# Kernel tuning notes

Hardware: AMD Instinct MI355X
Metric: run time of the kernel (lower is better)

## Reference

```python
import jax, jax.numpy as jnp
import numpy as np
import math

T, HW, M, D, DK, H, SIGMA = 16, 1024, 256, 768, 768, 8, 0.5
HD = DK // H
VHD = D // H
EPS = 1e-6
SCALE = 1.0 / math.sqrt(HD)


def _ln(x, g):
    # LayerNorm(eps=1e-6, bias=False)
    m = x.mean(-1, keepdims=True)
    v = ((x - m) ** 2).mean(-1, keepdims=True)
    return (x - m) / jnp.sqrt(v + EPS) * g


def setup_inputs() -> dict:
    key = jax.random.key(0)
    ks = jax.random.split(key, 16)
    s = 0.02
    features = jax.random.normal(ks[0], (T, HW, D), jnp.float32)
    tracks = jax.random.uniform(ks[1], (T, M, 2), jnp.float32)
    track_pos_embeddings = jax.random.normal(ks[2], (T, M, D), jnp.float32)
    feature_pos_embeddings = jax.random.normal(ks[3], (T, HW, D), jnp.float32)
    g = jnp.linspace(0.0, 1.0, 32)
    feature_positions = jnp.stack(jnp.meshgrid(g, g, indexing='ij'), axis=-1).reshape(HW, 2)
    return {
        'features': features,
        'tracks': tracks,
        'feature_positions': feature_positions,
        'track_pos_embeddings': track_pos_embeddings,
        'feature_pos_embeddings': feature_pos_embeddings,
        # AttentionalSampling params (nn.Linear weights are [out,in])
        'Wq_s': jax.random.normal(ks[4], (DK, D)) * s,
        'Wk_s': jax.random.normal(ks[5], (DK, D)) * s,
        'Wv_s': jax.random.normal(ks[6], (D, D)) * s,
        'qg_s': jnp.ones((DK,), jnp.float32),
        'kg_s': jnp.ones((DK,), jnp.float32),
        'Wo_s': jax.random.normal(ks[7], (D, D)) * s,
        # AttentionalSplatting params
        'Wq_p': jax.random.normal(ks[8], (DK, D)) * s,
        'Wk_p': jax.random.normal(ks[9], (DK, D)) * s,
        'Wv_p': jax.random.normal(ks[10], (D, D)) * s,
        'qg_p': jnp.ones((DK,), jnp.float32),
        'kg_p': jnp.ones((DK,), jnp.float32),
        'Wout_p': jax.random.normal(ks[11], (D, D)) * s,
    }


def reference(features, tracks, feature_positions, track_pos_embeddings,
              feature_pos_embeddings, Wq_s, Wk_s, Wv_s, qg_s, kg_s, Wo_s,
              Wq_p, Wk_p, Wv_p, qg_p, kg_p, Wout_p):
    # per-frame Gaussian spatial bias from squared euclidean distances
    # d2[t,m,n] = ||tracks[t,m] - feature_positions[n]||^2  -> [T, M, HW]
    d2 = ((tracks[:, :, None, :] - feature_positions[None, None, :, :]) ** 2).sum(-1)
    bias = -d2 / (2.0 * SIGMA ** 2)  # [T, M, HW]

    # ---- Attentional Sampling: tracks query features ----
    Q = _ln(track_pos_embeddings @ Wq_s.T, qg_s)          # [T, M, DK]
    K = _ln((features + feature_pos_embeddings) @ Wk_s.T, kg_s)  # [T, HW, DK]
    V = features @ Wv_s.T                                  # [T, HW, D]
    Qh = Q.reshape(T, M, H, HD).transpose(0, 2, 1, 3)      # [T, H, M, HD]
    Kh = K.reshape(T, HW, H, HD).transpose(0, 2, 1, 3)     # [T, H, HW, HD]
    Vh = V.reshape(T, HW, H, VHD).transpose(0, 2, 1, 3)    # [T, H, HW, VHD]
    scores = jnp.einsum('thmd,thnd->thmn', Qh, Kh) * SCALE + bias[:, None]
    A = jax.nn.softmax(scores, axis=-1)
    sampled = jnp.einsum('thmn,thnd->thmd', A, Vh)
    sampled = sampled.transpose(0, 2, 1, 3).reshape(T, M, D) @ Wo_s.T  # [T, M, D]

    # ---- Attentional Splatting: features query tracks ----
    Q2 = _ln(feature_pos_embeddings @ Wq_p.T, qg_p)        # [T, HW, DK]
    K2 = _ln(track_pos_embeddings @ Wk_p.T, kg_p)          # [T, M, DK]
    V2 = sampled @ Wv_p.T                                   # [T, M, D]
    Q2h = Q2.reshape(T, HW, H, HD).transpose(0, 2, 1, 3)   # [T, H, HW, HD]
    K2h = K2.reshape(T, M, H, HD).transpose(0, 2, 1, 3)    # [T, H, M, HD]
    V2h = V2.reshape(T, M, H, VHD).transpose(0, 2, 1, 3)   # [T, H, M, VHD]
    bias_t = jnp.swapaxes(bias, 1, 2)                       # [T, HW, M] (cdist is symmetric)
    scores2 = jnp.einsum('thnd,thmd->thnm', Q2h, K2h) * SCALE + bias_t[:, None]
    A2 = jax.nn.softmax(scores2, axis=-1)
    upd = jnp.einsum('thnm,thmd->thnd', A2, V2h)
    feature_updates = upd.transpose(0, 2, 1, 3).reshape(T, HW, D) @ Wout_p.T
    return features + feature_updates
```

## Files before the change

### kernel.cpp

```cpp
#include <hip/hip_runtime.h>

#define DD 768
#define HDIM 96
#define ATT_SCALE 0.10206207261596575f

typedef float floatx4 __attribute__((ext_vector_type(4)));
typedef __bf16 bf16;
typedef bf16 bf16x8 __attribute__((ext_vector_type(8)));
typedef bf16 bf16x4 __attribute__((ext_vector_type(4)));
typedef bf16 bf16x2 __attribute__((ext_vector_type(2)));

__device__ __forceinline__ void gl2lds16(const bf16* g, bf16* l) {
  __builtin_amdgcn_global_load_lds(
      (const __attribute__((address_space(1))) void*)g,
      (__attribute__((address_space(3))) void*)l, 16, 0, 0);
}

__global__ __launch_bounds__(256) void prep(
    const float* __restrict__ features, const float* __restrict__ fpe,
    const float* __restrict__ tpe,
    const float* w0, const float* w1, const float* w2, const float* w3,
    const float* w4, const float* w5, const float* w6, const float* w7,
    bf16* __restrict__ Fb, bf16* __restrict__ Xb, bf16* __restrict__ Feb,
    bf16* __restrict__ Tb, bf16* __restrict__ Wb, bf16* __restrict__ WoT) {
  const int b = blockIdx.x;
  const int tid = threadIdx.x;
  if (b < 6144) {
    const int i = (b * 256 + tid) * 8;
    floatx4 f0 = *(const floatx4*)(features + i);
    floatx4 f1 = *(const floatx4*)(features + i + 4);
    floatx4 e0 = *(const floatx4*)(fpe + i);
    floatx4 e1 = *(const floatx4*)(fpe + i + 4);
    bf16x8 fv, xv, ev;
#pragma unroll
    for (int k = 0; k < 4; k++) {
      fv[k] = (bf16)f0[k];           fv[k + 4] = (bf16)f1[k];
      ev[k] = (bf16)e0[k];           ev[k + 4] = (bf16)e1[k];
      xv[k] = (bf16)(f0[k] + e0[k]); xv[k + 4] = (bf16)(f1[k] + e1[k]);
    }
    *(bf16x8*)(Fb + i) = fv;
    *(bf16x8*)(Xb + i) = xv;
    *(bf16x8*)(Feb + i) = ev;
  } else if (b < 7680) {
    const int i = ((b - 6144) * 256 + tid) * 8;
    floatx4 s0 = *(const floatx4*)(tpe + i);
    floatx4 s1 = *(const floatx4*)(tpe + i + 4);
    bf16x8 v;
#pragma unroll
    for (int k = 0; k < 4; k++) { v[k] = (bf16)s0[k]; v[k + 4] = (bf16)s1[k]; }
    *(bf16x8*)(Tb + i) = v;
  } else if (b < 9984) {
    const int sub = b - 7680;
    const int wi = sub / 288, xb = sub % 288;
    const float* srcs[8] = {w0, w1, w2, w3, w4, w5, w6, w7};
    const float* s = srcs[wi];
    bf16* d = Wb + (size_t)wi * 589824;
    const int i = (xb * 256 + tid) * 8;
    floatx4 s0 = *(const floatx4*)(s + i);
    floatx4 s1 = *(const floatx4*)(s + i + 4);
    bf16x8 v;
#pragma unroll
    for (int k = 0; k < 4; k++) { v[k] = (bf16)s0[k]; v[k + 4] = (bf16)s1[k]; }
    *(bf16x8*)(d + i) = v;
  } else {
    __shared__ float Ts[64][65];
    const int sub = b - 9984;
    const int X0 = (sub % 12) * 64, Y0 = (sub / 12) * 64;
    const int r = tid >> 2;
    const int c4 = (tid & 3) * 16;
    const float* src = w3 + (size_t)(Y0 + r) * DD + X0 + c4;
#pragma unroll
    for (int k = 0; k < 16; k += 4) {
      floatx4 v = *(const floatx4*)(src + k);
      Ts[r][c4 + k] = v[0]; Ts[r][c4 + k + 1] = v[1];
      Ts[r][c4 + k + 2] = v[2]; Ts[r][c4 + k + 3] = v[3];
    }
    __syncthreads();
    bf16 o[16];
#pragma unroll
    for (int k = 0; k < 16; k++) o[k] = (bf16)Ts[c4 + k][r];
    *(bf16x8*)(WoT + (size_t)(X0 + r) * DD + Y0 + c4) = *(bf16x8*)&o[0];
    *(bf16x8*)(WoT + (size_t)(X0 + r) * DD + Y0 + c4 + 8) = *(bf16x8*)&o[8];
  }
}

__device__ __forceinline__ void ln_row(bf16* x, const float* g, int lane) {
  float v[12], s = 0.f, ss = 0.f;
#pragma unroll
  for (int j = 0; j < 3; j++) {
    bf16x4 b = *(const bf16x4*)&x[j * 256 + lane * 4];
#pragma unroll
    for (int e = 0; e < 4; e++) {
      float t = (float)b[e];
      v[j * 4 + e] = t; s += t; ss += t * t;
    }
  }
#pragma unroll
  for (int o = 32; o > 0; o >>= 1) { s += __shfl_xor(s, o); ss += __shfl_xor(ss, o); }
  const float mean = s * (1.0f / DD);
  const float inv = rsqrtf(ss * (1.0f / DD) - mean * mean + 1e-6f);
#pragma unroll
  for (int j = 0; j < 3; j++) {
    floatx4 gg = *(const floatx4*)&g[j * 256 + lane * 4];
    bf16x4 o4;
#pragma unroll
    for (int e = 0; e < 4; e++) o4[e] = (bf16)((v[j * 4 + e] - mean) * inv * gg[e]);
    *(bf16x4*)&x[j * 256 + lane * 4] = o4;
  }
}

__global__ __launch_bounds__(256) void ln_all(bf16* X0, const float* g0,
                                              bf16* X1, const float* g1,
                                              bf16* X2, const float* g2,
                                              bf16* X3, const float* g3) {
  const int b = blockIdx.x;
  bf16* X; const float* g; int base;
  if (b < 4096)      { X = X0; g = g0; base = b; }
  else if (b < 8192) { X = X1; g = g1; base = b - 4096; }
  else if (b < 9216) { X = X2; g = g2; base = b - 8192; }
  else               { X = X3; g = g3; base = b - 9216; }
  const int w = threadIdx.x >> 6, lane = threadIdx.x & 63;
  ln_row(X + (size_t)(base * 4 + w) * DD, g, lane);
}

template <int MODE>
__device__ __forceinline__ void gemm_core64(const bf16* __restrict__ A,
                                            const bf16* __restrict__ W,
                                            bf16* __restrict__ Cb,
                                            float* __restrict__ Cf,
                                            const float* __restrict__ addsrc,
                                            bf16* As, bf16* Ws,
                                            int row0, int col0) {
  const int tid = threadIdx.x;
  const int lane = tid & 63;
  const int w = tid >> 6;
  const int wm = (w & 1) * 64;
  const int wn = (w >> 1) * 64;
  const int fr = lane & 15;
  const int quad = lane >> 4;
  const int srow = tid >> 2;
  const int scol = (tid & 3) * 8;
  const bf16* Ag = A + (size_t)(row0 + srow) * DD + scol;
  const bf16* Wg = W + (size_t)(col0 + srow) * DD + scol;
  bf16* AsD = &As[tid * 8];
  bf16* WsD = &Ws[tid * 8];

  floatx4 acc[4][4];
#pragma unroll
  for (int i = 0; i < 4; i++)
#pragma unroll
    for (int j = 0; j < 4; j++) acc[i][j] = (floatx4){0, 0, 0, 0};

  for (int k0 = 0; k0 < DD; k0 += 64) {
    __syncthreads();
    gl2lds16(Ag + k0, AsD);
    gl2lds16(Ag + k0 + (size_t)64 * DD, AsD + 2048);
    gl2lds16(Wg + k0, WsD);
    gl2lds16(Wg + k0 + (size_t)64 * DD, WsD + 2048);
    gl2lds16(Ag + k0 + 32, AsD + 4096);
    gl2lds16(Ag + k0 + 32 + (size_t)64 * DD, AsD + 4096 + 2048);
    gl2lds16(Wg + k0 + 32, WsD + 4096);
    gl2lds16(Wg + k0 + 32 + (size_t)64 * DD, WsD + 4096 + 2048);
    __syncthreads();
#pragma unroll
    for (int half = 0; half < 2; half++) {
      const bf16* Ah = As + half * 4096;
      const bf16* Wh = Ws + half * 4096;
      bf16x8 af[4], bfr[4];
#pragma unroll
      for (int i = 0; i < 4; i++)
        af[i] = *(const bf16x8*)&Ah[(wm + i * 16 + fr) * 32 + quad * 8];
#pragma unroll
      for (int j = 0; j < 4; j++)
        bfr[j] = *(const bf16x8*)&Wh[(wn + j * 16 + fr) * 32 + quad * 8];
#pragma unroll
      for (int i = 0; i < 4; i++)
#pragma unroll
        for (int j = 0; j < 4; j++)
          acc[i][j] = __builtin_amdgcn_mfma_f32_16x16x32_bf16(af[i], bfr[j], acc[i][j], 0, 0, 0);
    }
  }
#pragma unroll
  for (int i = 0; i < 4; i++)
#pragma unroll
    for (int j = 0; j < 4; j++)
#pragma unroll
      for (int r = 0; r < 4; r++) {
        const int row = row0 + wm + i * 16 + quad * 4 + r;
        const int col = col0 + wn + j * 16 + fr;
        const size_t idx = (size_t)row * DD + col;
        if (MODE == 0) Cb[idx] = (bf16)acc[i][j][r];
        else Cf[idx] = acc[i][j][r] + addsrc[idx];
      }
}

__global__ __launch_bounds__(256) void gemm_all(
    const bf16* Xb, const bf16* Fb, const bf16* Feb, const bf16* Tb,
    const bf16* Wb, const bf16* WoT,
    bf16* Kc, bf16* Vc, bf16* Qb2, bf16* Qc, bf16* K2, bf16* Wcr) {
  __shared__ bf16 As[8192], Ws[8192];
  const size_t SW = (size_t)768 * 768;
  const int z = blockIdx.z;
  if (z == 0)
    gemm_core64<0>(Xb, Wb + 1 * SW, Kc, nullptr, nullptr, As, Ws,
                   blockIdx.x * 128, blockIdx.y * 128);
  else if (z == 1)
    gemm_core64<0>(Fb, Wb + 2 * SW, Vc, nullptr, nullptr, As, Ws,
                   blockIdx.x * 128, blockIdx.y * 128);
  else if (z == 2)
    gemm_core64<0>(Feb, Wb + 4 * SW, Qb2, nullptr, nullptr, As, Ws,
                   blockIdx.x * 128, blockIdx.y * 128);
  else {
    const int x = blockIdx.x;
    if (x < 32)
      gemm_core64<0>(Tb, Wb + 0 * SW, Qc, nullptr, nullptr, As, Ws,
                     x * 128, blockIdx.y * 128);
    else if (x < 64)
      gemm_core64<0>(Tb, Wb + 5 * SW, K2, nullptr, nullptr, As, Ws,
                     (x - 32) * 128, blockIdx.y * 128);
    else if (x < 70)
      gemm_core64<0>(Wb + 6 * SW, WoT, Wcr, nullptr, nullptr, As, Ws,
                     (x - 64) * 128, blockIdx.y * 128);
  }
}

__global__ __launch_bounds__(256) void gemm_b(const bf16* A, const bf16* W, bf16* C) {
  __shared__ bf16 As[8192], Ws[8192];
  gemm_core64<0>(A, W, C, nullptr, nullptr, As, Ws, blockIdx.x * 128, blockIdx.y * 128);
}

__global__ __launch_bounds__(256) void gemm_final(const bf16* A, const bf16* W,
                                                  float* C, const float* addsrc) {
  __shared__ bf16 As[8192], Ws[8192];
  gemm_core64<1>(A, W, nullptr, C, addsrc, As, Ws, blockIdx.x * 128, blockIdx.y * 128);
}

template <int SPLIT>
__global__ __launch_bounds__(512, 4) void attn512(
    const bf16* __restrict__ Qb, const bf16* __restrict__ Kb,
    const bf16* __restrict__ Vb, bf16* __restrict__ Ob,
    float* __restrict__ Ml,
    const float* __restrict__ qpos, int qpos_ts,
    const float* __restrict__ kpos, int kpos_ts,
    int nq, int nk, int npq, int nsp) {
  const int b = blockIdx.x;
  const int h = b & 7;
  const int t = (b >> 3) & 15;
  const int rest = b >> 7;
  const int qt = rest % npq;
  const int sp = rest / npq;
  const int klen = nk / nsp;
  const int k0s = sp * klen;
  const int q0 = qt * 128;
  const bf16* Q = Qb + (size_t)t * nq * DD + h * HDIM;
  const bf16* K = Kb + (size_t)t * nk * DD + h * HDIM;
  const bf16* V = Vb + (size_t)t * nk * DD + h * HDIM;
  bf16* O = Ob + (size_t)(SPLIT ? (sp * 16 + t) : t) * nq * DD + h * HDIM;
  const float* qp = qpos + (size_t)t * qpos_ts;
  const float* kp = kpos + (size_t)t * kpos_ts;

  __shared__ bf16 Ks[64 * 104];
  __shared__ bf16 Vt[96 * 72];
  __shared__ bf16 Ps[2 * 64 * 72];

  const int tid = threadIdx.x;
  const int w = tid >> 6;
  const int g = w >> 2;
  const int wl = w & 3;
  const int lane = tid & 63;
  const int fr = lane & 15;
  const int quad = lane >> 4;
  const int rowb = wl * 16;
  const int qgb = q0 + g * 64;
  bf16* Pg = &Ps[g * 64 * 72];

  bf16x8 qf[3];
  {
    const bf16* qrow = Q + (size_t)(qgb + rowb + fr) * DD;
#pragma unroll
    for (int c = 0; c < 3; c++) qf[c] = *(const bf16x8*)(qrow + c * 32 + quad * 8);
  }
  float qx[4], qy[4];
#pragma unroll
  for (int r = 0; r < 4; r++) {
    int qi = qgb + rowb + quad * 4 + r;
    qx[r] = qp[qi * 2];
    qy[r] = qp[qi * 2 + 1];
  }

  float lrow[4] = {0.f, 0.f, 0.f, 0.f};
  floatx4 oacc[6];
#pragma unroll
  for (int d = 0; d < 6; d++) oacc[d] = (floatx4){0, 0, 0, 0};

  const int krA = tid >> 3, kcA = (tid & 7) * 8;
  const int krB = (tid & 255) >> 2, kcB = 64 + (tid & 3) * 8;
  const int nb = (tid & 31) * 2, db = (tid >> 5) * 6;

  for (int n0 = k0s; n0 < k0s + klen; n0 += 64) {
    __syncthreads();
    *(bf16x8*)&Ks[krA * 104 + kcA] =
        *(const bf16x8*)(K + (size_t)(n0 + krA) * DD + kcA);
    if (tid < 256)
      *(bf16x8*)&Ks[krB * 104 + kcB] =
          *(const bf16x8*)(K + (size_t)(n0 + krB) * DD + kcB);
    {
      bf16 tmp[2][6];
#pragma unroll
      for (int nn = 0; nn < 2; nn++) {
        const unsigned* vg = (const unsigned*)(V + (size_t)(n0 + nb + nn) * DD + db);
        unsigned u0 = vg[0], u1 = vg[1], u2 = vg[2];
        *(unsigned*)&tmp[nn][0] = u0;
        *(unsigned*)&tmp[nn][2] = u1;
        *(unsigned*)&tmp[nn][4] = u2;
      }
#pragma unroll
      for (int dd = 0; dd < 6; dd++) {
        bf16x2 v2 = {tmp[0][dd], tmp[1][dd]};
        *(bf16x2*)&Vt[(db + dd) * 72 + nb] = v2;
      }
    }
    __syncthreads();

    floatx4 s4[4];
#pragma unroll
    for (int j = 0; j < 4; j++) {
      floatx4 sa = {0, 0, 0, 0};
#pragma unroll
      for (int c = 0; c < 3; c++) {
        bf16x8 kf = *(const bf16x8*)&Ks[(j * 16 + fr) * 104 + c * 32 + quad * 8];
        sa = __builtin_amdgcn_mfma_f32_16x16x32_bf16(qf[c], kf, sa, 0, 0, 0);
      }
      s4[j] = sa;
    }
    float kxx[4], kyy[4];
#pragma unroll
    for (int j = 0; j < 4; j++) {
      int ki = (n0 + j * 16 + fr) * 2;
      kxx[j] = kp[ki];
      kyy[j] = kp[ki + 1];
    }
#pragma unroll
    for (int j = 0; j < 4; j++)
#pragma unroll
      for (int r = 0; r < 4; r++) {
        float dx = qx[r] - kxx[j], dy = qy[r] - kyy[j];
        float sv = s4[j][r] * ATT_SCALE - 2.0f * (dx * dx + dy * dy);
        float pv = __expf(sv);
        lrow[r] += pv;
        Pg[(rowb + quad * 4 + r) * 72 + j * 16 + fr] = (bf16)pv;
      }
    bf16x8 pf0 = *(const bf16x8*)&Pg[(rowb + fr) * 72 + quad * 8];
    bf16x8 pf1 = *(const bf16x8*)&Pg[(rowb + fr) * 72 + 32 + quad * 8];
#pragma unroll
    for (int d = 0; d < 6; d++) {
      bf16x8 v0 = *(const bf16x8*)&Vt[(d * 16 + fr) * 72 + quad * 8];
      bf16x8 v1 = *(const bf16x8*)&Vt[(d * 16 + fr) * 72 + 32 + quad * 8];
      oacc[d] = __builtin_amdgcn_mfma_f32_16x16x32_bf16(pf0, v0, oacc[d], 0, 0, 0);
      oacc[d] = __builtin_amdgcn_mfma_f32_16x16x32_bf16(pf1, v1, oacc[d], 0, 0, 0);
    }
  }

#pragma unroll
  for (int r = 0; r < 4; r++)
#pragma unroll
    for (int o = 1; o < 16; o <<= 1) lrow[r] += __shfl_xor(lrow[r], o);

#pragma unroll
  for (int r = 0; r < 4; r++) {
    int row = qgb + rowb + quad * 4 + r;
    if (SPLIT) {
#pragma unroll
      for (int d = 0; d < 6; d++)
        O[(size_t)row * DD + d * 16 + fr] = (bf16)oacc[d][r];
      if (fr == 0)
        Ml[((size_t)(sp * 16 + t) * 8 + h) * nq + row] = lrow[r];
    } else {
      float inv = 1.0f / lrow[r];
#pragma unroll
      for (int d = 0; d < 6; d++)
        O[(size_t)row * DD + d * 16 + fr] = (bf16)(oacc[d][r] * inv);
    }
  }
}

__global__ __launch_bounds__(256) void combine4(const bf16* __restrict__ Op,
                                                const float* __restrict__ Ml,
                                                bf16* __restrict__ Out) {
  const int row = blockIdx.x;
  const int t = row >> 8;
  const int q = row & 255;
#pragma unroll
  for (int e = 0; e < 3; e++) {
    int dim = threadIdx.x + e * 256;
    int hh = dim / 96;
    float osum = 0.f, lsum = 0.f;
#pragma unroll
    for (int s = 0; s < 4; s++) {
      lsum += Ml[((size_t)(s * 16 + t) * 8 + hh) * 256 + q];
      osum += (float)Op[((size_t)(s * 16 + t) * 256 + q) * DD + dim];
    }
    Out[(size_t)row * DD + dim] = (bf16)(osum / lsum);
  }
}

extern "C" void kernel_launch(void* const* d_in, const int* in_sizes, int n_in,
                              void* d_out, int out_size, void* d_ws, size_t ws_size,
                              hipStream_t stream) {
  const float* features = (const float*)d_in[0];
  const float* tracks   = (const float*)d_in[1];
  const float* fpos     = (const float*)d_in[2];
  const float* tpe      = (const float*)d_in[3];
  const float* fpe      = (const float*)d_in[4];
  const float* Wq_s     = (const float*)d_in[5];
  const float* Wk_s     = (const float*)d_in[6];
  const float* Wv_s     = (const float*)d_in[7];
  const float* qg_s     = (const float*)d_in[8];
  const float* kg_s     = (const float*)d_in[9];
  const float* Wo_s     = (const float*)d_in[10];
  const float* Wq_p     = (const float*)d_in[11];
  const float* Wk_p     = (const float*)d_in[12];
  const float* Wv_p     = (const float*)d_in[13];
  const float* qg_p     = (const float*)d_in[14];
  const float* kg_p     = (const float*)d_in[15];
  const float* Wout_p   = (const float*)d_in[16];
  float* out = (float*)d_out;

  const size_t SB = (size_t)16 * 1024 * 768;
  const size_t SS = (size_t)16 * 256 * 768;
  const size_t SW = (size_t)768 * 768;
  bf16* p = (bf16*)d_ws;
  bf16* Fb  = p; p += SB;
  bf16* Xb  = p; p += SB;
  bf16* Feb = p; p += SB;
  bf16* Kc  = p; p += SB;
  bf16* Vc  = p; p += SB;
  bf16* Qb2 = p; p += SB;
  bf16* Tb  = p; p += SS;
  bf16* Qc  = p; p += SS;
  bf16* K2  = p; p += SS;
  bf16* Sh  = p; p += SS;
  bf16* Op  = p; p += 4 * SS;
  bf16* Wb  = p; p += 8 * SW;
  bf16* WoT = p; p += SW;
  bf16* Wcr = p; p += SW;
  float* Ml = (float*)p;
  bf16* V2 = Qc; bf16* U = Fb;

  dim3 blk(256);

  prep<<<10128, blk, 0, stream>>>(features, fpe, tpe,
                                  Wq_s, Wk_s, Wv_s, Wo_s, Wq_p, Wk_p, Wv_p, Wout_p,
                                  Fb, Xb, Feb, Tb, Wb, WoT);
  gemm_all<<<dim3(128, 6, 4), blk, 0, stream>>>(Xb, Fb, Feb, Tb, Wb, WoT,
                                                Kc, Vc, Qb2, Qc, K2, Wcr);
  ln_all<<<10240, blk, 0, stream>>>(Kc, kg_s, Qb2, qg_p, Qc, qg_s, K2, kg_p);
  attn512<1><<<1024, dim3(512), 0, stream>>>(Qc, Kc, Vc, Op, Ml,
                                             tracks, 512, fpos, 0, 256, 1024, 2, 4);
  combine4<<<4096, blk, 0, stream>>>(Op, Ml, Sh);
  gemm_b<<<dim3(32, 6), blk, 0, stream>>>(Sh, Wcr, V2);
  attn512<0><<<1024, dim3(512), 0, stream>>>(Qb2, K2, V2, U, nullptr,
                                             fpos, 0, tracks, 512, 1024, 256, 8, 1);
  gemm_final<<<dim3(128, 6), blk, 0, stream>>>(U, Wb + 7 * SW, out, features);
}
```

Before: 474.4 us.

## Replace 128x128 GEMM core with 256x256 double-buffered, swizzled 8-wave pipeline

Replaces the shared GEMM routine with a 256x256 output tile computed by 512 threads (8 waves). It double-buffers LDS staging with direct global-to-LDS loads and XOR-swizzles the LDS layout to avoid bank conflicts. An explicitly interleaved schedule of LDS fragment reads, MFMA bursts, barriers, vmcnt waits and setprio is meant to overlap global prefetch with matrix math and raise operand reuse per byte loaded. The cost is 128KB of LDS per block, so likely one block per CU, and far fewer blocks per GEMM (e.g. 192 for the final projection). That can leave CUs idle and gives less latency hiding from occupancy.

New measurement: 440.1 us. 1.08x faster.

```diff
diff --git a/kernel.cpp b/kernel.cpp
--- a/kernel.cpp
+++ b/kernel.cpp
@@ -123,116 +123,189 @@
   ln_row(X + (size_t)(base * 4 + w) * DD, g, lane);
 }
 
+#define BAR() do { __builtin_amdgcn_sched_barrier(0); \
+                   __builtin_amdgcn_s_barrier(); \
+                   __builtin_amdgcn_sched_barrier(0); } while (0)
+#define VMW(n) asm volatile("s_waitcnt vmcnt(" #n ")" ::: "memory")
+
 template <int MODE>
-__device__ __forceinline__ void gemm_core64(const bf16* __restrict__ A,
-                                            const bf16* __restrict__ W,
-                                            bf16* __restrict__ Cb,
-                                            float* __restrict__ Cf,
-                                            const float* __restrict__ addsrc,
-                                            bf16* As, bf16* Ws,
-                                            int row0, int col0) {
+__device__ __forceinline__ void gemm256(const bf16* __restrict__ A,
+                                        const bf16* __restrict__ W,
+                                        bf16* __restrict__ Cb,
+                                        float* __restrict__ Cf,
+                                        const float* __restrict__ addsrc,
+                                        bf16* lds, int row0, int col0) {
   const int tid = threadIdx.x;
   const int lane = tid & 63;
   const int w = tid >> 6;
-  const int wm = (w & 1) * 64;
+  const int wm = (w & 1) * 128;
   const int wn = (w >> 1) * 64;
   const int fr = lane & 15;
   const int quad = lane >> 4;
-  const int srow = tid >> 2;
-  const int scol = (tid & 3) * 8;
-  const bf16* Ag = A + (size_t)(row0 + srow) * DD + scol;
-  const bf16* Wg = W + (size_t)(col0 + srow) * DD + scol;
-  bf16* AsD = &As[tid * 8];
-  bf16* WsD = &Ws[tid * 8];
-
-  floatx4 acc[4][4];
-#pragma unroll
-  for (int i = 0; i < 4; i++)
+  const int f7 = fr & 7;
+
+  const int srow = tid >> 3;
+  const int sswz = ((tid & 7) ^ (srow & 7)) * 8;
+  const bf16* Ag = A + (size_t)(row0 + srow) * DD + sswz;
+  const bf16* Wg = W + (size_t)(col0 + srow) * DD + sswz;
+  bf16* dA = lds + tid * 8;
+  bf16* dB = lds + 32768 + tid * 8;
+
+#define STGA(tau, h) do { \
+    gl2lds16(Ag + (size_t)((h) * 128) * DD + (tau) * 64, \
+             dA + ((tau) & 1) * 16384 + (h) * 8192); \
+    gl2lds16(Ag + (size_t)((h) * 128 + 64) * DD + (tau) * 64, \
+             dA + ((tau) & 1) * 16384 + (h) * 8192 + 4096); \
+  } while (0)
+#define STGB(tau, h) do { \
+    gl2lds16(Wg + (size_t)((h) * 128) * DD + (tau) * 64, \
+             dB + ((tau) & 1) * 16384 + (h) * 8192); \
+    gl2lds16(Wg + (size_t)((h) * 128 + 64) * DD + (tau) * 64, \
+             dB + ((tau) & 1) * 16384 + (h) * 8192 + 4096); \
+  } while (0)
+
+  const int sl0 = (quad ^ f7) * 8;
+  const int sl1 = ((4 | quad) ^ f7) * 8;
+
+#define LDA8(buf, mh) do { \
+    _Pragma("unroll") for (int m = 0; m < 4; m++) { \
+      const bf16* p = lds + (buf) * 16384 + (wm + (mh) * 64 + m * 16 + fr) * 64; \
+      af[m][0] = *(const bf16x8*)(p + sl0); \
+      af[m][1] = *(const bf16x8*)(p + sl1); } \
+  } while (0)
+#define LDB4(buf, nh, dst) do { \
+    _Pragma("unroll") for (int n = 0; n < 2; n++) { \
+      const bf16* p = lds + 32768 + (buf) * 16384 + (wn + (nh) * 32 + n * 16 + fr) * 64; \
+      dst[n][0] = *(const bf16x8*)(p + sl0); \
+      dst[n][1] = *(const bf16x8*)(p + sl1); } \
+  } while (0)
+#define MM16(mh, nbase, bb) do { \
+    __builtin_amdgcn_s_setprio(1); \
+    _Pragma("unroll") for (int m = 0; m < 4; m++) \
+    _Pragma("unroll") for (int n = 0; n < 2; n++) { \
+      acc[(mh) * 4 + m][(nbase) + n] = __builtin_amdgcn_mfma_f32_16x16x32_bf16( \
+          af[m][0], bb[n][0], acc[(mh) * 4 + m][(nbase) + n], 0, 0, 0); \
+      acc[(mh) * 4 + m][(nbase) + n] = __builtin_amdgcn_mfma_f32_16x16x32_bf16( \
+          af[m][1], bb[n][1], acc[(mh) * 4 + m][(nbase) + n], 0, 0, 0); } \
+    __builtin_amdgcn_s_setprio(0); \
+  } while (0)
+
+  floatx4 acc[8][4];
+
+  STGB(0, 0); STGB(0, 1); STGA(0, 0); STGA(0, 1);
+  STGB(1, 0); STGB(1, 1);
+#pragma unroll
+  for (int i = 0; i < 8; i++)
 #pragma unroll
     for (int j = 0; j < 4; j++) acc[i][j] = (floatx4){0, 0, 0, 0};
-
-  for (int k0 = 0; k0 < DD; k0 += 64) {
-    __syncthreads();
-    gl2lds16(Ag + k0, AsD);
-    gl2lds16(Ag + k0 + (size_t)64 * DD, AsD + 2048);
-    gl2lds16(Wg + k0, WsD);
-    gl2lds16(Wg + k0 + (size_t)64 * DD, WsD + 2048);
-    gl2lds16(Ag + k0 + 32, AsD + 4096);
-    gl2lds16(Ag + k0 + 32 + (size_t)64 * DD, AsD + 4096 + 2048);
-    gl2lds16(Wg + k0 + 32, WsD + 4096);
-    gl2lds16(Wg + k0 + 32 + (size_t)64 * DD, WsD + 4096 + 2048);
-    __syncthreads();
-#pragma unroll
-    for (int half = 0; half < 2; half++) {
-      const bf16* Ah = As + half * 4096;
-      const bf16* Wh = Ws + half * 4096;
-      bf16x8 af[4], bfr[4];
-#pragma unroll
-      for (int i = 0; i < 4; i++)
-        af[i] = *(const bf16x8*)&Ah[(wm + i * 16 + fr) * 32 + quad * 8];
-#pragma unroll
-      for (int j = 0; j < 4; j++)
-        bfr[j] = *(const bf16x8*)&Wh[(wn + j * 16 + fr) * 32 + quad * 8];
-#pragma unroll
-      for (int i = 0; i < 4; i++)
-#pragma unroll
-        for (int j = 0; j < 4; j++)
-          acc[i][j] = __builtin_amdgcn_mfma_f32_16x16x32_bf16(af[i], bfr[j], acc[i][j], 0, 0, 0);
-    }
-  }
-#pragma unroll
-  for (int i = 0; i < 4; i++)
-#pragma unroll
-    for (int j = 0; j < 4; j++)
+  VMW(4);
+  BAR();
+
+  bf16x8 af[4][2], b0[2][2], b1[2][2];
+
+  for (int it = 0; it < 6; ++it) {
+    const int a = 2 * it;
+    const bool stg = (it < 5);
+    LDA8(0, 0); LDB4(0, 0, b0);
+    STGA(a + 1, 0);
+    BAR();
+    MM16(0, 0, b0);
+    BAR();
+    LDB4(0, 1, b1);
+    STGA(a + 1, 1);
+    BAR();
+    MM16(0, 2, b1);
+    BAR();
+    LDA8(0, 1);
+    if (stg) STGB(a + 2, 0);
+    BAR();
+    MM16(1, 2, b1);
+    BAR();
+    if (stg) STGB(a + 2, 1);
+    BAR();
+    MM16(1, 0, b0);
+    if (stg) { VMW(4); } else { VMW(0); }
+    BAR();
+    LDA8(1, 0); LDB4(1, 0, b0);
+    if (stg) STGA(a + 2, 0);
+    BAR();
+    MM16(0, 0, b0);
+    BAR();
+    LDB4(1, 1, b1);
+    if (stg) STGA(a + 2, 1);
+    BAR();
+    MM16(0, 2, b1);
+    BAR();
+    LDA8(1, 1);
+    if (stg) STGB(a + 3, 0);
+    BAR();
+    MM16(1, 2, b1);
+    BAR();
+    if (stg) STGB(a + 3, 1);
+    BAR();
+    MM16(1, 0, b0);
+    if (stg) VMW(4);
+    BAR();
+  }
+
+#pragma unroll
+  for (int m = 0; m < 8; m++)
+#pragma unroll
+    for (int n = 0; n < 4; n++)
 #pragma unroll
       for (int r = 0; r < 4; r++) {
-        const int row = row0 + wm + i * 16 + quad * 4 + r;
-        const int col = col0 + wn + j * 16 + fr;
+        const int row = row0 + wm + m * 16 + quad * 4 + r;
+        const int col = col0 + wn + n * 16 + fr;
         const size_t idx = (size_t)row * DD + col;
-        if (MODE == 0) Cb[idx] = (bf16)acc[i][j][r];
-        else Cf[idx] = acc[i][j][r] + addsrc[idx];
+        if (MODE == 0) Cb[idx] = (bf16)acc[m][n][r];
+        else Cf[idx] = acc[m][n][r] + addsrc[idx];
       }
-}
-
-__global__ __launch_bounds__(256) void gemm_all(
+#undef STGA
+#undef STGB
+#undef LDA8
+#undef LDB4
+#undef MM16
+}
+
+__global__ __launch_bounds__(512, 2) void gemm_all(
     const bf16* Xb, const bf16* Fb, const bf16* Feb, const bf16* Tb,
     const bf16* Wb, const bf16* WoT,
     bf16* Kc, bf16* Vc, bf16* Qb2, bf16* Qc, bf16* K2, bf16* Wcr) {
-  __shared__ bf16 As[8192], Ws[8192];
+  __shared__ bf16 lds[65536];
   const size_t SW = (size_t)768 * 768;
   const int z = blockIdx.z;
   if (z == 0)
-    gemm_core64<0>(Xb, Wb + 1 * SW, Kc, nullptr, nullptr, As, Ws,
-                   blockIdx.x * 128, blockIdx.y * 128);
+    gemm256<0>(Xb, Wb + 1 * SW, Kc, nullptr, nullptr, lds,
+               blockIdx.x * 256, blockIdx.y * 256);
   else if (z == 1)
-    gemm_core64<0>(Fb, Wb + 2 * SW, Vc, nullptr, nullptr, As, Ws,
-                   blockIdx.x * 128, blockIdx.y * 128);
+    gemm256<0>(Fb, Wb + 2 * SW, Vc, nullptr, nullptr, lds,
+               blockIdx.x * 256, blockIdx.y * 256);
   else if (z == 2)
-    gemm_core64<0>(Feb, Wb + 4 * SW, Qb2, nullptr, nullptr, As, Ws,
-                   blockIdx.x * 128, blockIdx.y * 128);
+    gemm256<0>(Feb, Wb + 4 * SW, Qb2, nullptr, nullptr, lds,
+               blockIdx.x * 256, blockIdx.y * 256);
   else {
     const int x = blockIdx.x;
-    if (x < 32)
-      gemm_core64<0>(Tb, Wb + 0 * SW, Qc, nullptr, nullptr, As, Ws,
-                     x * 128, blockIdx.y * 128);
-    else if (x < 64)
-      gemm_core64<0>(Tb, Wb + 5 * SW, K2, nullptr, nullptr, As, Ws,
-                     (x - 32) * 128, blockIdx.y * 128);
-    else if (x < 70)
-      gemm_core64<0>(Wb + 6 * SW, WoT, Wcr, nullptr, nullptr, As, Ws,
-                     (x - 64) * 128, blockIdx.y * 128);
-  }
-}
-
-__global__ __launch_bounds__(256) void gemm_b(const bf16* A, const bf16* W, bf16* C) {
-  __shared__ bf16 As[8192], Ws[8192];
-  gemm_core64<0>(A, W, C, nullptr, nullptr, As, Ws, blockIdx.x * 128, blockIdx.y * 128);
-}
-
-__global__ __launch_bounds__(256) void gemm_final(const bf16* A, const bf16* W,
-                                                  float* C, const float* addsrc) {
-  __shared__ bf16 As[8192], Ws[8192];
-  gemm_core64<1>(A, W, nullptr, C, addsrc, As, Ws, blockIdx.x * 128, blockIdx.y * 128);
+    if (x < 16)
+      gemm256<0>(Tb, Wb + 0 * SW, Qc, nullptr, nullptr, lds,
+                 x * 256, blockIdx.y * 256);
+    else if (x < 32)
+      gemm256<0>(Tb, Wb + 5 * SW, K2, nullptr, nullptr, lds,
+                 (x - 16) * 256, blockIdx.y * 256);
+    else if (x < 35)
+      gemm256<0>(Wb + 6 * SW, WoT, Wcr, nullptr, nullptr, lds,
+                 (x - 32) * 256, blockIdx.y * 256);
+  }
+}
+
+__global__ __launch_bounds__(512, 2) void gemm_b(const bf16* A, const bf16* W, bf16* C) {
+  __shared__ bf16 lds[65536];
+  gemm256<0>(A, W, C, nullptr, nullptr, lds, blockIdx.x * 256, blockIdx.y * 256);
+}
+
+__global__ __launch_bounds__(512, 2) void gemm_final(const bf16* A, const bf16* W,
+                                                     float* C, const float* addsrc) {
+  __shared__ bf16 lds[65536];
+  gemm256<1>(A, W, nullptr, C, addsrc, lds, blockIdx.x * 256, blockIdx.y * 256);
 }
 
 template <int SPLIT>
@@ -452,14 +525,14 @@
   prep<<<10128, blk, 0, stream>>>(features, fpe, tpe,
                                   Wq_s, Wk_s, Wv_s, Wo_s, Wq_p, Wk_p, Wv_p, Wout_p,
                                   Fb, Xb, Feb, Tb, Wb, WoT);
-  gemm_all<<<dim3(128, 6, 4), blk, 0, stream>>>(Xb, Fb, Feb, Tb, Wb, WoT,
-                                                Kc, Vc, Qb2, Qc, K2, Wcr);
+  gemm_all<<<dim3(64, 3, 4), dim3(512), 0, stream>>>(Xb, Fb, Feb, Tb, Wb, WoT,
+                                                     Kc, Vc, Qb2, Qc, K2, Wcr);
   ln_all<<<10240, blk, 0, stream>>>(Kc, kg_s, Qb2, qg_p, Qc, qg_s, K2, kg_p);
   attn512<1><<<1024, dim3(512), 0, stream>>>(Qc, Kc, Vc, Op, Ml,
                                              tracks, 512, fpos, 0, 256, 1024, 2, 4);
   combine4<<<4096, blk, 0, stream>>>(Op, Ml, Sh);
-  gemm_b<<<dim3(32, 6), blk, 0, stream>>>(Sh, Wcr, V2);
+  gemm_b<<<dim3(16, 3), dim3(512), 0, stream>>>(Sh, Wcr, V2);
   attn512<0><<<1024, dim3(512), 0, stream>>>(Qb2, K2, V2, U, nullptr,
                                              fpos, 0, tracks, 512, 1024, 256, 8, 1);
-  gemm_final<<<dim3(128, 6), blk, 0, stream>>>(U, Wb + 7 * SW, out, features);
-}
+  gemm_final<<<dim3(64, 3), dim3(512), 0, stream>>>(U, Wb + 7 * SW, out, features);
+}
```
